# Kernel tuning notes

Measured on AMD Instinct MI355X. Metric: run time of the kernel, lower is better.

## Reference

```python
import jax, jax.numpy as jnp
import numpy as np

B, N, C = 128, 36, 1024
K_NB = 16            # neighbors per node (top-k, includes loop)
KERNEL = 8           # number of Gaussian kernels
OUT = 1024           # out_dim; per-kernel out = OUT // KERNEL
PI = np.float32(np.pi)


def setup_inputs() -> dict:
    key = jax.random.key(0)
    ks = jax.random.split(key, 9)
    node_feats = jax.random.normal(ks[0], (B, N, C), dtype=jnp.float32)
    node_centre = jax.random.uniform(ks[1], (B, N, 2), dtype=jnp.float32)
    neighbor_idx = jax.random.randint(ks[2], (B * N, K_NB), 0, B * N, dtype=jnp.int32)
    graph_weights = jax.random.uniform(ks[3], (B * N * K_NB, 1), dtype=jnp.float32)
    # Gaussian kernel params (per reset_parameters)
    mean_rho = jax.random.uniform(ks[4], (1, KERNEL), dtype=jnp.float32)
    mean_theta = jax.random.uniform(ks[5], (1, KERNEL), minval=-PI, maxval=PI, dtype=jnp.float32)
    precision_rho = jax.random.uniform(ks[6], (1, KERNEL), minval=0.5, maxval=1.0, dtype=jnp.float32)
    precision_theta = jax.random.uniform(ks[7], (1, KERNEL), minval=0.5, maxval=1.0, dtype=jnp.float32)
    # per-kernel Linear(node_dim, out_dim//kernel, bias=False), stacked: [K, d_out_k, C]
    conv_w = jax.random.normal(ks[8], (KERNEL, OUT // KERNEL, C), dtype=jnp.float32) * (1.0 / np.sqrt(C))
    return {
        "node_feats": node_feats,
        "node_centre": node_centre,
        "neighbor_idx": neighbor_idx,
        "graph_weights": graph_weights,
        "mean_rho": mean_rho,
        "mean_theta": mean_theta,
        "precision_rho": precision_rho,
        "precision_theta": precision_theta,
        "conv_w": conv_w,
    }


def _forward(node_feats, node_centre, graph_weights,
             mean_rho, mean_theta, precision_rho, precision_theta,
             conv_w, neighbor_idx):
    b, n, c = node_feats.shape
    bn = b * n
    # pseudo polar coordinates per edge: centre_i - centre_j
    centre = node_centre.reshape(bn, 2)                       # [BN, 2]
    diff = centre[:, None, :] - centre[neighbor_idx]          # [BN, K_nb, 2]
    coord_x = diff[..., 0].reshape(-1)                        # [E]
    coord_y = diff[..., 1].reshape(-1)
    rho = jnp.sqrt(coord_x ** 2 + coord_y ** 2)
    theta = jnp.arctan2(coord_x, coord_y)
    # Gaussian mixture membership weights over KERNEL kernels
    w_rho = jnp.exp(-0.5 * (rho[:, None] - mean_rho) ** 2 / (1e-14 + precision_rho ** 2))
    first_angle = jnp.abs(theta[:, None] - mean_theta)
    second_angle = jnp.abs(2.0 * PI - first_angle)
    w_theta = jnp.exp(-0.5 * jnp.minimum(first_angle, second_angle) ** 2 / (1e-14 + precision_theta ** 2))
    weights = w_rho * w_theta                                  # [E, KERNEL]
    weights = jnp.where(jnp.isnan(weights), 0.0, weights)
    weights = weights / jnp.sum(weights, axis=1, keepdims=True)
    # combine with graph edge weights
    edge_w = graph_weights * weights                           # [E, KERNEL]
    edge_w = edge_w.reshape(bn, K_NB, KERNEL).transpose(0, 2, 1)  # [BN, K, K_nb]
    # gather neighbor features and weighted aggregate (bmm)
    nbr = node_feats.reshape(bn, c)[neighbor_idx]              # [BN, K_nb, C]
    agg = jnp.einsum('ekn,enc->ekc', edge_w, nbr)              # [BN, KERNEL, C]
    agg = agg.reshape(b, n, KERNEL, c)
    # per-kernel linear then concat over kernel dim
    out = jnp.einsum('bnkc,kdc->bnkd', agg, conv_w)            # [B, N, KERNEL, OUT//KERNEL]
    out = out.reshape(b, n, -1)                                # [B, N, OUT]
    return jax.nn.relu(out)


def reference(node_feats, node_centre, neighbor_idx, graph_weights,
              mean_rho, mean_theta, precision_rho, precision_theta, conv_w):
    return _forward(node_feats, node_centre, graph_weights,
                    mean_rho, mean_theta, precision_rho, precision_theta,
                    conv_w, neighbor_idx)
```

## Files before the change

### kernel.cpp

```cpp
#include <hip/hip_runtime.h>
#include <hip/hip_bf16.h>
#include <stdint.h>

#define B_DIM   128
#define N_DIM   36
#define C_DIM   1024
#define KNB     16
#define NKER    8
#define OUTD    1024
#define BN_NODES (B_DIM * N_DIM)
#define E_EDGES  (BN_NODES * KNB)
#define PI_F 3.14159265358979323846f

#define TM 48
#define TN 128
#define BK 64
#define KIT (C_DIM / BK)
#define CLP 136
#define A_OFF(p) ((p) * TM * BK)
#define B_OFF(p) (2 * TM * BK + (p) * TN * BK)

typedef __attribute__((ext_vector_type(8))) short bf16x8;
typedef __attribute__((ext_vector_type(4))) float floatx4;

struct alignas(8)  U16x4 { unsigned short x, y, z, w; };
struct alignas(16) U16x8 { unsigned short s[8]; };

__device__ __forceinline__ unsigned short f2bf(float f) {
  union { float f; uint32_t u; } v; v.f = f;
  uint32_t u = v.u;
  return (unsigned short)((u + 0x7fffu + ((u >> 16) & 1u)) >> 16);
}
__device__ __forceinline__ float bf2f_lo(uint32_t pair) {
  union { uint32_t u; float f; } v; v.u = pair << 16;
  return v.f;
}
__device__ __forceinline__ float bf2f_hi(uint32_t pair) {
  union { uint32_t u; float f; } v; v.u = pair & 0xffff0000u;
  return v.f;
}

__device__ __forceinline__ void gload16(const void* g, void* l) {
  __builtin_amdgcn_global_load_lds((__attribute__((address_space(1))) void*)(g),
                                   (__attribute__((address_space(3))) void*)(l),
                                   16, 0, 0);
}

__global__ __launch_bounds__(256)
void castw_ew_kernel(const float* __restrict__ cw,
                     const float* __restrict__ centre,
                     const int*   __restrict__ nbr,
                     const float* __restrict__ gw,
                     const float* __restrict__ mrho,
                     const float* __restrict__ mth,
                     const float* __restrict__ prho,
                     const float* __restrict__ pth,
                     unsigned short* __restrict__ wb,
                     float* __restrict__ ewg)
{
  const int NW4 = (C_DIM * OUTD) / 4;
  int tid = blockIdx.x * 256 + threadIdx.x;
  if (tid < NW4) {
    float4 v = ((const float4*)cw)[tid];
    U16x4 o = { f2bf(v.x), f2bf(v.y), f2bf(v.z), f2bf(v.w) };
    ((U16x4*)wb)[tid] = o;
  } else {
    int e = tid - NW4;
    if (e < E_EDGES) {
      int n = e >> 4;
      int m = nbr[e];
      float cx = centre[2 * n]     - centre[2 * m];
      float cy = centre[2 * n + 1] - centre[2 * m + 1];
      float rho   = sqrtf(cx * cx + cy * cy);
      float theta = atan2f(cx, cy);
      float wk[NKER];
      float s = 0.f;
#pragma unroll
      for (int k = 0; k < NKER; ++k) {
        float dr = rho - mrho[k];
        float pr = prho[k];
        float w_r = expf(-0.5f * dr * dr / (1e-14f + pr * pr));
        float fa = fabsf(theta - mth[k]);
        float sa = fabsf(2.0f * PI_F - fa);
        float mm = fminf(fa, sa);
        float pt = pth[k];
        float w_t = expf(-0.5f * mm * mm / (1e-14f + pt * pt));
        float ww = w_r * w_t;
        wk[k] = (ww != ww) ? 0.f : ww;
        s += wk[k];
      }
      float scale = gw[e] / s;
      int j = e & 15;
#pragma unroll
      for (int k = 0; k < NKER; ++k)
        ewg[(size_t)n * (NKER * KNB) + k * KNB + j] = wk[k] * scale;
    }
  }
}

__global__ __launch_bounds__(256)
void gemm_fused(const float* __restrict__ A,
                const unsigned short* __restrict__ Bt,
                unsigned short* __restrict__ D)
{
  __shared__ unsigned short smem[2 * TM * BK + 2 * TN * BK];

  const int tid  = threadIdx.x;
  const int lane = tid & 63;
  const int wv   = tid >> 6;
  const int row0 = blockIdx.x * TM;
  const int col0 = blockIdx.y * TN;

  const int q  = lane >> 4;
  const int lr = lane & 15;

  floatx4 acc[3][2] = {};

  int offB[4];
#pragma unroll
  for (int i = 0; i < 4; ++i) {
    int c = tid + 256 * i, row = c >> 3, qc = c & 7;
    offB[i] = (col0 + row) * C_DIM + (qc ^ (row & 7)) * 8;
  }

  const int r0A = tid >> 3;
  const int gA0 = (row0 + r0A) * C_DIM + (tid & 7) * 8;
  const int r2A = 32 + (tid >> 4);
  const int gA2 = (row0 + r2A) * C_DIM + (tid & 15) * 4;
  const int wA0 = r0A * BK + (((tid & 7) ^ (r0A & 7)) * 8);
  const int wA2 = r2A * BK + ((((tid >> 1) & 7) ^ (r2A & 7)) * 8) + (tid & 1) * 4;

  float4 a0, a1, a2;

#define LOADA(T) do {                                                        \
    a0 = *(const float4*)&A[gA0 + (T) * BK];                                 \
    a1 = *(const float4*)&A[gA0 + 4 + (T) * BK];                             \
    a2 = *(const float4*)&A[gA2 + (T) * BK];                                 \
  } while (0)

#define WRITEA(P) do {                                                       \
    U16x8 w8;                                                                \
    w8.s[0] = f2bf(a0.x); w8.s[1] = f2bf(a0.y);                              \
    w8.s[2] = f2bf(a0.z); w8.s[3] = f2bf(a0.w);                              \
    w8.s[4] = f2bf(a1.x); w8.s[5] = f2bf(a1.y);                              \
    w8.s[6] = f2bf(a1.z); w8.s[7] = f2bf(a1.w);                              \
    *(U16x8*)&smem[A_OFF(P) + wA0] = w8;                                     \
    U16x4 w4 = { f2bf(a2.x), f2bf(a2.y), f2bf(a2.z), f2bf(a2.w) };           \
    *(U16x4*)&smem[A_OFF(P) + wA2] = w4;                                     \
  } while (0)

#define DMAB(T, P) do {                                                      \
    _Pragma("unroll") for (int i = 0; i < 4; ++i)                            \
      gload16(Bt + offB[i] + (T) * BK,                                       \
              &smem[B_OFF(P) + (tid + 256 * i) * 8]);                        \
  } while (0)

  LOADA(0);
  DMAB(0, 0);
  WRITEA(0);
  __syncthreads();

  for (int t = 0; t < KIT; ++t) {
    const int p = t & 1;
    if (t + 1 < KIT) { DMAB(t + 1, 1 - p); LOADA(t + 1); }

    const int aBase = A_OFF(p);
    const int bBase = B_OFF(p);
#pragma unroll
    for (int kc = 0; kc < 2; ++kc) {
      const int sc = ((kc * 4 + q) ^ (lr & 15 & 7)) * 8;
      bf16x8 af[3], bfr[2];
#pragma unroll
      for (int i = 0; i < 3; ++i)
        af[i]  = *(const bf16x8*)&smem[aBase + (i * 16 + lr) * BK + sc];
#pragma unroll
      for (int j = 0; j < 2; ++j)
        bfr[j] = *(const bf16x8*)&smem[bBase + (wv * 32 + j * 16 + lr) * BK + sc];
#pragma unroll
      for (int i = 0; i < 3; ++i)
#pragma unroll
        for (int j = 0; j < 2; ++j)
          acc[i][j] = __builtin_amdgcn_mfma_f32_16x16x32_bf16(
              af[i], bfr[j], acc[i][j], 0, 0, 0);
    }

    if (t + 1 < KIT) WRITEA(1 - p);
    __syncthreads();
  }
#undef LOADA
#undef WRITEA
#undef DMAB

#pragma unroll
  for (int i = 0; i < 3; ++i)
#pragma unroll
    for (int j = 0; j < 2; ++j)
#pragma unroll
      for (int r = 0; r < 4; ++r)
        smem[(i * 16 + q * 4 + r) * CLP + wv * 32 + j * 16 + lr] =
            f2bf(acc[i][j][r]);
  __syncthreads();
#pragma unroll
  for (int i = 0; i < 3; ++i) {
    int c = tid + 256 * i;
    int row = c >> 4, qc = c & 15;
    *(uint4*)&D[(size_t)(row0 + row) * OUTD + col0 + qc * 8] =
        *(const uint4*)&smem[row * CLP + qc * 8];
  }
}

__global__ __launch_bounds__(256)
void agg_gather(const unsigned short* __restrict__ proj,
                const int*   __restrict__ nbr,
                const float* __restrict__ ewg,
                float* __restrict__ out)
{
  __shared__ int   idx[8][KNB];
  __shared__ float ewl[8][2][KNB];

  const int bid = blockIdx.x;
  const int x   = bid & 7;
  const int s   = x >> 1;
  const int g   = ((bid >> 3) << 1) | (x & 1);
  const int n0  = g * 8;
  const int t   = threadIdx.x;

  if (t < 128)
    idx[t >> 4][t & 15] = nbr[(n0 + (t >> 4)) * KNB + (t & 15)];
  {
    int a = t >> 5, r = t & 31;
    ewl[a][r >> 4][r & 15] = ewg[(size_t)(n0 + a) * (NKER * KNB) + s * 32 + r];
  }
  __syncthreads();

  const int a   = t >> 5;
  const int cu  = t & 31;
  const int kk  = cu >> 4;
  const int n   = n0 + a;
  const int ch0 = s * 256 + cu * 8;

  float acc[8] = {0.f, 0.f, 0.f, 0.f, 0.f, 0.f, 0.f, 0.f};
#pragma unroll
  for (int j = 0; j < KNB; ++j) {
    float wvv = ewl[a][kk][j];
    uint4 v = *(const uint4*)&proj[(size_t)idx[a][j] * OUTD + ch0];
    acc[0] += wvv * bf2f_lo(v.x);  acc[1] += wvv * bf2f_hi(v.x);
    acc[2] += wvv * bf2f_lo(v.y);  acc[3] += wvv * bf2f_hi(v.y);
    acc[4] += wvv * bf2f_lo(v.z);  acc[5] += wvv * bf2f_hi(v.z);
    acc[6] += wvv * bf2f_lo(v.w);  acc[7] += wvv * bf2f_hi(v.w);
  }
  float4 r0, r1;
  r0.x = fmaxf(acc[0], 0.f); r0.y = fmaxf(acc[1], 0.f);
  r0.z = fmaxf(acc[2], 0.f); r0.w = fmaxf(acc[3], 0.f);
  r1.x = fmaxf(acc[4], 0.f); r1.y = fmaxf(acc[5], 0.f);
  r1.z = fmaxf(acc[6], 0.f); r1.w = fmaxf(acc[7], 0.f);
  float* o = out + (size_t)n * OUTD + ch0;
  *(float4*)(o)     = r0;
  *(float4*)(o + 4) = r1;
}

extern "C" void kernel_launch(void* const* d_in, const int* in_sizes, int n_in,
                              void* d_out, int out_size, void* d_ws, size_t ws_size,
                              hipStream_t stream)
{
  const float* feats  = (const float*)d_in[0];
  const float* centre = (const float*)d_in[1];
  const int*   nbr    = (const int*)  d_in[2];
  const float* gw     = (const float*)d_in[3];
  const float* mrho   = (const float*)d_in[4];
  const float* mth    = (const float*)d_in[5];
  const float* prho   = (const float*)d_in[6];
  const float* pth    = (const float*)d_in[7];
  const float* cw     = (const float*)d_in[8];
  float* out = (float*)d_out;

  char* ws = (char*)d_ws;
  unsigned short* wb   = (unsigned short*)(ws);
  unsigned short* proj = (unsigned short*)(ws + 2097152);
  float*          ewg  = (float*)         (ws + 11534336);

  const int NW4 = (C_DIM * OUTD) / 4;
  const int EWB = (E_EDGES + 255) / 256;
  castw_ew_kernel<<<dim3(NW4 / 256 + EWB), dim3(256), 0, stream>>>(
      cw, centre, nbr, gw, mrho, mth, prho, pth, wb, ewg);
  gemm_fused<<<dim3(BN_NODES / TM, OUTD / TN), dim3(256), 0, stream>>>(
      feats, wb, proj);
  agg_gather<<<dim3(BN_NODES / 2), dim3(256), 0, stream>>>(proj, nbr, ewg, out);
}
```

Measured before the change: 121.6 us.

## Load B operand directly into registers instead of staging through LDS

The weight (B) tile is no longer DMA'd into shared memory with global_load_lds. Each wave now loads its own B fragments straight from global memory into registers, double-buffered across two register sets, with the loop unrolled by two. This shrinks LDS usage to the A buffers plus the epilogue tile and removes the LDS reads for B. In exchange it adds register pressure, and the global loads are less coalesced (16-byte per-lane rows), with no reuse of B across the four waves. Each wave reads a distinct column range, so there is no redundant traffic.

```diff
diff --git a/kernel.cpp b/kernel.cpp
--- a/kernel.cpp
+++ b/kernel.cpp
@@ -18,7 +18,6 @@
 #define KIT (C_DIM / BK)
 #define CLP 136
 #define A_OFF(p) ((p) * TM * BK)
-#define B_OFF(p) (2 * TM * BK + (p) * TN * BK)
 
 typedef __attribute__((ext_vector_type(8))) short bf16x8;
 typedef __attribute__((ext_vector_type(4))) float floatx4;
@@ -38,12 +37,6 @@
 __device__ __forceinline__ float bf2f_hi(uint32_t pair) {
   union { uint32_t u; float f; } v; v.u = pair & 0xffff0000u;
   return v.f;
-}
-
-__device__ __forceinline__ void gload16(const void* g, void* l) {
-  __builtin_amdgcn_global_load_lds((__attribute__((address_space(1))) void*)(g),
-                                   (__attribute__((address_space(3))) void*)(l),
-                                   16, 0, 0);
 }
 
 __global__ __launch_bounds__(256)
@@ -103,7 +96,7 @@
                 const unsigned short* __restrict__ Bt,
                 unsigned short* __restrict__ D)
 {
-  __shared__ unsigned short smem[2 * TM * BK + 2 * TN * BK];
+  __shared__ unsigned short smem[6528];
 
   const int tid  = threadIdx.x;
   const int lane = tid & 63;
@@ -116,12 +109,10 @@
 
   floatx4 acc[3][2] = {};
 
-  int offB[4];
-#pragma unroll
-  for (int i = 0; i < 4; ++i) {
-    int c = tid + 256 * i, row = c >> 3, qc = c & 7;
-    offB[i] = (col0 + row) * C_DIM + (qc ^ (row & 7)) * 8;
-  }
+  int bB[2];
+#pragma unroll
+  for (int j = 0; j < 2; ++j)
+    bB[j] = (col0 + wv * 32 + j * 16 + lr) * C_DIM + q * 8;
 
   const int r0A = tid >> 3;
   const int gA0 = (row0 + r0A) * C_DIM + (tid & 7) * 8;
@@ -149,47 +140,44 @@
     *(U16x4*)&smem[A_OFF(P) + wA2] = w4;                                     \
   } while (0)
 
-#define DMAB(T, P) do {                                                      \
-    _Pragma("unroll") for (int i = 0; i < 4; ++i)                            \
-      gload16(Bt + offB[i] + (T) * BK,                                       \
-              &smem[B_OFF(P) + (tid + 256 * i) * 8]);                        \
-  } while (0)
+#define LOADB(T, BN_) do {                                                   \
+    _Pragma("unroll") for (int kc = 0; kc < 2; ++kc)                         \
+      _Pragma("unroll") for (int j = 0; j < 2; ++j)                          \
+        BN_[kc][j] = *(const bf16x8*)&Bt[bB[j] + (T) * BK + kc * 32];        \
+  } while (0)
+
+#define PHASE(T, P, BC, BN_) do {                                            \
+    if ((T) + 1 < KIT) { LOADB((T) + 1, BN_); LOADA((T) + 1); }              \
+    const int aBase = A_OFF(P);                                              \
+    _Pragma("unroll") for (int kc = 0; kc < 2; ++kc) {                       \
+      const int sc = ((kc * 4 + q) ^ (lr & 7)) * 8;                          \
+      bf16x8 af[3];                                                          \
+      _Pragma("unroll") for (int i = 0; i < 3; ++i)                          \
+        af[i] = *(const bf16x8*)&smem[aBase + (i * 16 + lr) * BK + sc];      \
+      _Pragma("unroll") for (int i = 0; i < 3; ++i)                          \
+        _Pragma("unroll") for (int j = 0; j < 2; ++j)                        \
+          acc[i][j] = __builtin_amdgcn_mfma_f32_16x16x32_bf16(               \
+              af[i], BC[kc][j], acc[i][j], 0, 0, 0);                         \
+    }                                                                        \
+    if ((T) + 1 < KIT) WRITEA(1 - (P));                                      \
+    __syncthreads();                                                         \
+  } while (0)
+
+  bf16x8 bX[2][2], bY[2][2];
 
   LOADA(0);
-  DMAB(0, 0);
+  LOADB(0, bX);
   WRITEA(0);
   __syncthreads();
 
-  for (int t = 0; t < KIT; ++t) {
-    const int p = t & 1;
-    if (t + 1 < KIT) { DMAB(t + 1, 1 - p); LOADA(t + 1); }
-
-    const int aBase = A_OFF(p);
-    const int bBase = B_OFF(p);
-#pragma unroll
-    for (int kc = 0; kc < 2; ++kc) {
-      const int sc = ((kc * 4 + q) ^ (lr & 15 & 7)) * 8;
-      bf16x8 af[3], bfr[2];
-#pragma unroll
-      for (int i = 0; i < 3; ++i)
-        af[i]  = *(const bf16x8*)&smem[aBase + (i * 16 + lr) * BK + sc];
-#pragma unroll
-      for (int j = 0; j < 2; ++j)
-        bfr[j] = *(const bf16x8*)&smem[bBase + (wv * 32 + j * 16 + lr) * BK + sc];
-#pragma unroll
-      for (int i = 0; i < 3; ++i)
-#pragma unroll
-        for (int j = 0; j < 2; ++j)
-          acc[i][j] = __builtin_amdgcn_mfma_f32_16x16x32_bf16(
-              af[i], bfr[j], acc[i][j], 0, 0, 0);
-    }
-
-    if (t + 1 < KIT) WRITEA(1 - p);
-    __syncthreads();
+  for (int t = 0; t < KIT; t += 2) {
+    PHASE(t,     0, bX, bY);
+    PHASE(t + 1, 1, bY, bX);
   }
 #undef LOADA
 #undef WRITEA
-#undef DMAB
+#undef LOADB
+#undef PHASE
 
 #pragma unroll
   for (int i = 0; i < 3; ++i)
```

After: 131.7 us. 8.3% more time.

## Double GEMM row tile to 96 with 2x2 wave grid and XCD-aware block mapping

Applied to the files above, without the earlier changes.

Raises the GEMM M-tile from 48 to 96 rows and arranges the four waves as a 2x2 grid, each computing 48x64, so every B tile loaded into shared memory is reused across twice as many rows. The grid becomes 1-D, and each block index is remapped so consecutive row blocks land on the same XCD for better L2 locality. The cost is more accumulator registers per thread, a larger shared-memory A buffer, and half as many blocks, which may reduce occupancy and load balance across CUs.

```diff
diff --git a/kernel.cpp b/kernel.cpp
--- a/kernel.cpp
+++ b/kernel.cpp
@@ -12,7 +12,7 @@
 #define E_EDGES  (BN_NODES * KNB)
 #define PI_F 3.14159265358979323846f
 
-#define TM 48
+#define TM 96
 #define TN 128
 #define BK 64
 #define KIT (C_DIM / BK)
@@ -24,7 +24,6 @@
 typedef __attribute__((ext_vector_type(4))) float floatx4;
 
 struct alignas(8)  U16x4 { unsigned short x, y, z, w; };
-struct alignas(16) U16x8 { unsigned short s[8]; };
 
 __device__ __forceinline__ unsigned short f2bf(float f) {
   union { float f; uint32_t u; } v; v.f = f;
@@ -107,14 +106,20 @@
 
   const int tid  = threadIdx.x;
   const int lane = tid & 63;
-  const int wv   = tid >> 6;
-  const int row0 = blockIdx.x * TM;
-  const int col0 = blockIdx.y * TN;
+  const int wave = tid >> 6;
+  const int wm   = wave >> 1;
+  const int wn   = wave & 1;
+
+  const int bid  = blockIdx.x;
+  const int xcd  = bid & 7;
+  const int rb   = bid >> 3;
+  const int row0 = (xcd * 6 + (rb % 6)) * TM;
+  const int col0 = (rb / 6) * TN;
 
   const int q  = lane >> 4;
   const int lr = lane & 15;
 
-  floatx4 acc[3][2] = {};
+  floatx4 acc[3][4] = {};
 
   int offB[4];
 #pragma unroll
@@ -123,30 +128,26 @@
     offB[i] = (col0 + row) * C_DIM + (qc ^ (row & 7)) * 8;
   }
 
-  const int r0A = tid >> 3;
-  const int gA0 = (row0 + r0A) * C_DIM + (tid & 7) * 8;
-  const int r2A = 32 + (tid >> 4);
-  const int gA2 = (row0 + r2A) * C_DIM + (tid & 15) * 4;
-  const int wA0 = r0A * BK + (((tid & 7) ^ (r0A & 7)) * 8);
-  const int wA2 = r2A * BK + ((((tid >> 1) & 7) ^ (r2A & 7)) * 8) + (tid & 1) * 4;
-
-  float4 a0, a1, a2;
+  int gA[6], wA[6];
+#pragma unroll
+  for (int i = 0; i < 6; ++i) {
+    int c = tid + 256 * i, row = c >> 4, f4 = c & 15;
+    gA[i] = (row0 + row) * C_DIM + f4 * 4;
+    wA[i] = row * BK + (((f4 >> 1) ^ (row & 7)) * 8) + (f4 & 1) * 4;
+  }
+
+  float4 a[6];
 
 #define LOADA(T) do {                                                        \
-    a0 = *(const float4*)&A[gA0 + (T) * BK];                                 \
-    a1 = *(const float4*)&A[gA0 + 4 + (T) * BK];                             \
-    a2 = *(const float4*)&A[gA2 + (T) * BK];                                 \
+    _Pragma("unroll") for (int i = 0; i < 6; ++i)                            \
+      a[i] = *(const float4*)&A[gA[i] + (T) * BK];                           \
   } while (0)
 
 #define WRITEA(P) do {                                                       \
-    U16x8 w8;                                                                \
-    w8.s[0] = f2bf(a0.x); w8.s[1] = f2bf(a0.y);                              \
-    w8.s[2] = f2bf(a0.z); w8.s[3] = f2bf(a0.w);                              \
-    w8.s[4] = f2bf(a1.x); w8.s[5] = f2bf(a1.y);                              \
-    w8.s[6] = f2bf(a1.z); w8.s[7] = f2bf(a1.w);                              \
-    *(U16x8*)&smem[A_OFF(P) + wA0] = w8;                                     \
-    U16x4 w4 = { f2bf(a2.x), f2bf(a2.y), f2bf(a2.z), f2bf(a2.w) };           \
-    *(U16x4*)&smem[A_OFF(P) + wA2] = w4;                                     \
+    _Pragma("unroll") for (int i = 0; i < 6; ++i) {                          \
+      U16x4 w4 = { f2bf(a[i].x), f2bf(a[i].y), f2bf(a[i].z), f2bf(a[i].w) }; \
+      *(U16x4*)&smem[A_OFF(P) + wA[i]] = w4;                                 \
+    }                                                                        \
   } while (0)
 
 #define DMAB(T, P) do {                                                      \
@@ -168,18 +169,18 @@
     const int bBase = B_OFF(p);
 #pragma unroll
     for (int kc = 0; kc < 2; ++kc) {
-      const int sc = ((kc * 4 + q) ^ (lr & 15 & 7)) * 8;
-      bf16x8 af[3], bfr[2];
+      const int sc = ((kc * 4 + q) ^ (lr & 7)) * 8;
+      bf16x8 af[3], bfr[4];
 #pragma unroll
       for (int i = 0; i < 3; ++i)
-        af[i]  = *(const bf16x8*)&smem[aBase + (i * 16 + lr) * BK + sc];
-#pragma unroll
-      for (int j = 0; j < 2; ++j)
-        bfr[j] = *(const bf16x8*)&smem[bBase + (wv * 32 + j * 16 + lr) * BK + sc];
+        af[i]  = *(const bf16x8*)&smem[aBase + (wm * 48 + i * 16 + lr) * BK + sc];
+#pragma unroll
+      for (int j = 0; j < 4; ++j)
+        bfr[j] = *(const bf16x8*)&smem[bBase + (wn * 64 + j * 16 + lr) * BK + sc];
 #pragma unroll
       for (int i = 0; i < 3; ++i)
 #pragma unroll
-        for (int j = 0; j < 2; ++j)
+        for (int j = 0; j < 4; ++j)
           acc[i][j] = __builtin_amdgcn_mfma_f32_16x16x32_bf16(
               af[i], bfr[j], acc[i][j], 0, 0, 0);
     }
@@ -194,14 +195,14 @@
 #pragma unroll
   for (int i = 0; i < 3; ++i)
 #pragma unroll
-    for (int j = 0; j < 2; ++j)
+    for (int j = 0; j < 4; ++j)
 #pragma unroll
       for (int r = 0; r < 4; ++r)
-        smem[(i * 16 + q * 4 + r) * CLP + wv * 32 + j * 16 + lr] =
+        smem[(wm * 48 + i * 16 + q * 4 + r) * CLP + wn * 64 + j * 16 + lr] =
             f2bf(acc[i][j][r]);
   __syncthreads();
 #pragma unroll
-  for (int i = 0; i < 3; ++i) {
+  for (int i = 0; i < 6; ++i) {
     int c = tid + 256 * i;
     int row = c >> 4, qc = c & 15;
     *(uint4*)&D[(size_t)(row0 + row) * OUTD + col0 + qc * 8] =
@@ -283,7 +284,7 @@
   const int EWB = (E_EDGES + 255) / 256;
   castw_ew_kernel<<<dim3(NW4 / 256 + EWB), dim3(256), 0, stream>>>(
       cw, centre, nbr, gw, mrho, mth, prho, pth, wb, ewg);
-  gemm_fused<<<dim3(BN_NODES / TM, OUTD / TN), dim3(256), 0, stream>>>(
+  gemm_fused<<<dim3((BN_NODES / TM) * (OUTD / TN)), dim3(256), 0, stream>>>(
       feats, wb, proj);
   agg_gather<<<dim3(BN_NODES / 2), dim3(256), 0, stream>>>(proj, nbr, ewg, out);
 }
```

New measurement: 122.9 us. No clear change (+1.0%).
